# Optimization experiments

Hardware: AMD Instinct MI355X
Metric: run time of the kernel (lower is better)

The kernel has to match this reference:

```python
import jax, jax.numpy as jnp
import numpy as np

N = 50000
E = 1600000
INPUT_DIM = 128
HEADS = 4
OUT_DIM = 32
LRELU_ALPHA = 0.2


def setup_inputs() -> dict:
    key = jax.random.key(0)
    k1, k2, k3, k4, k5 = jax.random.split(key, 5)
    gain = 1.0 / (1.0 + LRELU_ALPHA)
    input_proj = jax.random.normal(k1, (N, INPUT_DIM), dtype=jnp.float32)
    edge_index = jax.random.randint(k2, (2, E), 0, N, dtype=jnp.int64)
    W = jax.random.normal(k3, (INPUT_DIM, HEADS * OUT_DIM), dtype=jnp.float32) * (gain / INPUT_DIM) ** 0.5
    A_left = jax.random.normal(k4, (HEADS, OUT_DIM, 1), dtype=jnp.float32) * (gain / OUT_DIM)
    A_right = jax.random.normal(k5, (HEADS, OUT_DIM, 1), dtype=jnp.float32) * (gain / OUT_DIM)
    return {"input_proj": input_proj, "edge_index": edge_index, "W": W, "A_left": A_left, "A_right": A_right}


def reference(input_proj, edge_index, W, A_left, A_right):
    n = input_proj.shape[0]
    heads, out_dim = A_left.shape[0], A_left.shape[1]
    # Linear projection: [N, heads, out_dim]
    H = (input_proj @ W).reshape(n, heads, out_dim)
    # Per-node attention scores: [N, heads]
    H_s = jnp.einsum('nhd,hd->nh', H, A_left[..., 0])
    H_t = jnp.einsum('nhd,hd->nh', H, A_right[..., 0])
    src = edge_index[0]
    tgt = edge_index[1]
    # Edge scores: leaky_relu(H_s[src] + H_t[tgt]) -> [E, heads]
    e = H_s[src] + H_t[tgt]
    e = jnp.where(e > 0, e, LRELU_ALPHA * e)
    # Segment softmax over neighborhoods keyed by source node (global max shift, as in original)
    e = jnp.exp(e - jnp.max(e))
    denom = jax.ops.segment_sum(e, src, num_segments=n)  # [N, heads]
    alpha = e / (denom[src] + 1e-8)
    # Weighted scatter-add aggregation of target features: [N, heads, out_dim]
    msg = alpha[:, :, None] * H[tgt]
    agg = jax.ops.segment_sum(msg, src, num_segments=n)
    # concat_last=True -> [N, heads*out_dim], then ELU
    res = agg.reshape(n, heads * out_dim)
    return jax.nn.elu(res)
```

## Files before the change

### kernel.cpp

```cpp
#include <hip/hip_runtime.h>

#define DIM 128
#define HEADS 4
#define ODIM 32
#define LRELU 0.2f
#define PT 4096
#define CAP 9216

typedef unsigned int u32;
typedef unsigned short u16;
typedef unsigned char u8;

typedef __attribute__((ext_vector_type(8))) short bf16x8;
typedef __attribute__((ext_vector_type(4))) float f32x4;

__device__ __forceinline__ u16 f2bf(float f) {
    union { u32 u; float f; } x; x.f = f;
    u32 u = x.u;
    u32 r = u + 0x7FFFu + ((u >> 16) & 1u);
    return (u16)(r >> 16);
}
__device__ __forceinline__ float blo(u32 b) {
    union { u32 u; float f; } x; x.u = b << 16; return x.f;
}
__device__ __forceinline__ float bhi(u32 b) {
    union { u32 u; float f; } x; x.u = b & 0xFFFF0000u; return x.f;
}

__global__ __launch_bounds__(256) void prep_kernel(
    const float* __restrict__ W, u16* __restrict__ Wt, int* __restrict__ bcur)
{
    __shared__ u16 s[128 * 136];
    int t = threadIdx.x;
    bcur[t] = t * CAP;
    for (int i = 0; i < 64; ++i) {
        int idx = i * 256 + t;
        int k = idx >> 7, nn = idx & 127;
        s[nn * 136 + k] = f2bf(W[idx]);
    }
    __syncthreads();
    for (int i = 0; i < 64; ++i) {
        int idx = i * 256 + t;
        int nn = idx >> 7, k = idx & 127;
        Wt[idx] = s[nn * 136 + k];
    }
}

__global__ __launch_bounds__(256) void proj_kernel(
    const float* __restrict__ X, const u16* __restrict__ Wt,
    const float* __restrict__ AL, const float* __restrict__ AR,
    u32* __restrict__ Hb, float* __restrict__ Hs, float* __restrict__ Ht, int n)
{
    __shared__ alignas(16) float sH[64 * 132];
    __shared__ float sAL[DIM], sAR[DIM];
    const int t = threadIdx.x;
    if (t < DIM) { sAL[t] = AL[t]; sAR[t] = AR[t]; }
    const int row0 = blockIdx.x * 64;
    const int w = t >> 6, lane = t & 63;
    const int quad = lane >> 4, nIdx = lane & 15;
    const int m = row0 + w * 16 + nIdx;

    f32x4 acc[8];
    #pragma unroll
    for (int c = 0; c < 8; ++c) acc[c] = (f32x4){0.f, 0.f, 0.f, 0.f};

    #pragma unroll
    for (int kq = 0; kq < 4; ++kq) {
        union { bf16x8 v; u16 e[8]; } a;
        if (m < n) {
            const float* xp = &X[(size_t)m * DIM + kq * 32 + quad * 8];
            float4 x0 = *(const float4*)xp;
            float4 x1 = *(const float4*)(xp + 4);
            a.e[0] = f2bf(x0.x); a.e[1] = f2bf(x0.y);
            a.e[2] = f2bf(x0.z); a.e[3] = f2bf(x0.w);
            a.e[4] = f2bf(x1.x); a.e[5] = f2bf(x1.y);
            a.e[6] = f2bf(x1.z); a.e[7] = f2bf(x1.w);
        } else {
            #pragma unroll
            for (int j = 0; j < 8; ++j) a.e[j] = 0;
        }
        #pragma unroll
        for (int c = 0; c < 8; ++c) {
            bf16x8 b = *(const bf16x8*)&Wt[(c * 16 + nIdx) * DIM + kq * 32 + quad * 8];
            acc[c] = __builtin_amdgcn_mfma_f32_16x16x32_bf16(a.v, b, acc[c], 0, 0, 0);
        }
    }
    #pragma unroll
    for (int c = 0; c < 8; ++c)
        #pragma unroll
        for (int r = 0; r < 4; ++r)
            sH[(w * 16 + quad * 4 + r) * 132 + c * 16 + nIdx] = acc[c][r];
    __syncthreads();

    #pragma unroll
    for (int i = 0; i < 16; ++i) {
        int idx = i * 256 + t;
        int r = idx >> 6, d2 = idx & 63;
        int gr = row0 + r;
        if (gr < n) {
            float2 hv = *(const float2*)&sH[r * 132 + 2 * d2];
            Hb[(size_t)gr * 64 + d2] = ((u32)f2bf(hv.y) << 16) | (u32)f2bf(hv.x);
        }
    }
    {
        int r = t >> 2, h = t & 3;
        float s = 0.f, s2 = 0.f;
        #pragma unroll
        for (int q = 0; q < ODIM; q += 4) {
            float4 hv = *(const float4*)&sH[r * 132 + h * ODIM + q];
            s  += hv.x*sAL[h*ODIM+q] + hv.y*sAL[h*ODIM+q+1] + hv.z*sAL[h*ODIM+q+2] + hv.w*sAL[h*ODIM+q+3];
            s2 += hv.x*sAR[h*ODIM+q] + hv.y*sAR[h*ODIM+q+1] + hv.z*sAR[h*ODIM+q+2] + hv.w*sAR[h*ODIM+q+3];
        }
        int gr = row0 + r;
        if (gr < n) { Hs[gr * HEADS + h] = s; Ht[gr * HEADS + h] = s2; }
    }
}

__device__ __forceinline__ int scan256_excl(int v, int t, int* wsum) {
    int lane = t & 63, w = t >> 6;
    int inc = v;
    #pragma unroll
    for (int ofs = 1; ofs < 64; ofs <<= 1) {
        int x = __shfl_up(inc, ofs);
        if (lane >= ofs) inc += x;
    }
    __syncthreads();
    if (lane == 63) wsum[w] = inc;
    __syncthreads();
    int add = 0;
    #pragma unroll
    for (int j = 0; j < 4; ++j) add += (j < w) ? wsum[j] : 0;
    return inc - v + add;
}

__global__ __launch_bounds__(256) void partition_kernel(
    const int* __restrict__ ei, int* __restrict__ bcur,
    u32* __restrict__ part, int E, int n)
{
    __shared__ u32 stage[PT];
    __shared__ u8  sbkt[PT];
    __shared__ int lcnt4[4][256];
    __shared__ int lcur4[4][256];
    __shared__ int loff[256], ltot[256], gbase[256];
    __shared__ int wsum[4];
    const int t = threadIdx.x;
    const int wv = t >> 6;
    const int base = blockIdx.x * PT;
    lcnt4[0][t] = 0; lcnt4[1][t] = 0; lcnt4[2][t] = 0; lcnt4[3][t] = 0;
    __syncthreads();

    u32 key[16];
    int bkt[16];
    #pragma unroll
    for (int i = 0; i < 16; ++i) {
        int e = base + i * 256 + t;
        bkt[i] = -1;
        key[i] = 0;
        if (e < E) {
            int src = ei[e];
            int tgt = ei[E + e];
            src = max(0, min(src, n - 1));
            tgt = max(0, min(tgt, n - 1));
            bkt[i] = src >> 8;
            key[i] = ((u32)(src & 255) << 17) | (u32)tgt;
            atomicAdd(&lcnt4[wv][bkt[i]], 1);
        }
    }
    __syncthreads();
    int c0 = lcnt4[0][t], c1 = lcnt4[1][t], c2 = lcnt4[2][t], c3 = lcnt4[3][t];
    int total = c0 + c1 + c2 + c3;
    int ex = scan256_excl(total, t, wsum);
    loff[t] = ex;
    ltot[t] = total;
    lcur4[0][t] = ex;
    lcur4[1][t] = ex + c0;
    lcur4[2][t] = ex + c0 + c1;
    lcur4[3][t] = ex + c0 + c1 + c2;
    gbase[t] = (total > 0) ? atomicAdd(&bcur[t], total) : 0;
    __syncthreads();
    #pragma unroll
    for (int i = 0; i < 16; ++i) {
        if (bkt[i] >= 0) {
            int p = atomicAdd(&lcur4[wv][bkt[i]], 1);
            stage[p] = key[i];
            sbkt[p] = (u8)bkt[i];
        }
    }
    __syncthreads();
    int tot = loff[255] + ltot[255];
    for (int i = t; i < tot; i += 256) {
        int b = sbkt[i];
        int dst = gbase[b] + (i - loff[b]);
        if (dst < (b + 1) * CAP) part[dst] = stage[i];
    }
}

__global__ __launch_bounds__(256) void csrfill_kernel(
    const u32* __restrict__ part, const int* __restrict__ bcur,
    int* __restrict__ off, int* __restrict__ csr_tgt, int n, int ntiles)
{
    __shared__ int lc4[4][256];
    __shared__ int lcur4[4][256];
    __shared__ int lo[256];
    __shared__ int wsum[4];
    __shared__ int sBase, sCnt;
    const int b = blockIdx.x, t = threadIdx.x;
    const int wv = t >> 6;
    int myc = (t < ntiles) ? (bcur[t] - t * CAP) : 0;
    myc = max(0, min(myc, CAP));
    int ex = scan256_excl(myc, t, wsum);
    if (t == b) { sBase = ex; sCnt = myc; }
    lc4[0][t] = 0; lc4[1][t] = 0; lc4[2][t] = 0; lc4[3][t] = 0;
    __syncthreads();
    const int pbase = b * CAP;
    const int base = sBase, cnt = sCnt;
    for (int i = t; i < cnt; i += 256)
        atomicAdd(&lc4[wv][part[pbase + i] >> 17], 1);
    __syncthreads();
    int c0 = lc4[0][t], c1 = lc4[1][t], c2 = lc4[2][t], c3 = lc4[3][t];
    int total = c0 + c1 + c2 + c3;
    int ex2 = scan256_excl(total, t, wsum);
    lo[t] = ex2;
    lcur4[0][t] = ex2;
    lcur4[1][t] = ex2 + c0;
    lcur4[2][t] = ex2 + c0 + c1;
    lcur4[3][t] = ex2 + c0 + c1 + c2;
    __syncthreads();
    int node = b * 256 + t;
    if (node < n) off[node] = base + lo[t];
    if (b == ntiles - 1 && t == 0) off[n] = base + cnt;
    for (int i = t; i < cnt; i += 256) {
        u32 key = part[pbase + i];
        int p = atomicAdd(&lcur4[wv][key >> 17], 1);
        csr_tgt[base + p] = (int)(key & 0x1FFFFu);
    }
}

__global__ __launch_bounds__(256) void agg_kernel(
    const u32* __restrict__ Hb, const float* __restrict__ Hs,
    const float* __restrict__ Ht, const int* __restrict__ off,
    const int* __restrict__ csr_tgt, float2* __restrict__ out, int n, int E)
{
    int node = (blockIdx.x * 256 + threadIdx.x) >> 6;
    int L = threadIdx.x & 63;
    if (node >= n) return;
    int lo = off[node], hi = off[node + 1];
    lo = max(0, min(lo, E));
    hi = max(lo, min(hi, E));
    const int h = L >> 4;
    const int eSel = (L & 31) >> 2;
    const int hSel = L & 3;
    float4 hs4 = *(const float4*)&Hs[node * HEADS];
    float hsC = hSel == 0 ? hs4.x : hSel == 1 ? hs4.y : hSel == 2 ? hs4.z : hs4.w;
    float hsO = h == 0 ? hs4.x : h == 1 ? hs4.y : h == 2 ? hs4.z : hs4.w;
    float ax = 0.f, ay = 0.f, Sd = 0.f, Srem = 0.f;

    int i = lo;
    for (; i + 8 <= hi; i += 8) {
        int tt[8];
        #pragma unroll
        for (int j = 0; j < 8; ++j) tt[j] = csr_tgt[i + j];
        int tsel = csr_tgt[i + eSel];
        float e = hsC + Ht[tsel * HEADS + hSel];
        float w = __expf(fminf(e > 0.f ? e : LRELU * e, 30.f));
        Sd += w;
        u32 bb[8];
        #pragma unroll
        for (int j = 0; j < 8; ++j) bb[j] = Hb[tt[j] * 64 + L];
        #pragma unroll
        for (int j = 0; j < 8; ++j) {
            float wj = __shfl(w, (j << 2) | h);
            ax += wj * blo(bb[j]);
            ay += wj * bhi(bb[j]);
        }
    }
    for (; i < hi; ++i) {
        int tgt = csr_tgt[i];
        float e = hsO + Ht[tgt * HEADS + h];
        float w = __expf(fminf(e > 0.f ? e : LRELU * e, 30.f));
        u32 b = Hb[tgt * 64 + L];
        ax += w * blo(b);
        ay += w * bhi(b);
        Srem += w;
    }
    float S = Srem;
    #pragma unroll
    for (int j = 0; j < 8; ++j) S += __shfl(Sd, (j << 2) | h);
    float inv = 1.f / (S + 1e-8f);
    float ox = ax * inv, oy = ay * inv;
    ox = ox > 0.f ? ox : (__expf(ox) - 1.f);
    oy = oy > 0.f ? oy : (__expf(oy) - 1.f);
    out[(size_t)node * 64 + L] = {ox, oy};
}

extern "C" void kernel_launch(void* const* d_in, const int* in_sizes, int n_in,
                              void* d_out, int out_size, void* d_ws, size_t ws_size,
                              hipStream_t stream) {
    const float* X  = (const float*)d_in[0];
    const int*   EI = (const int*)d_in[1];
    const float* W  = (const float*)d_in[2];
    const float* AL = (const float*)d_in[3];
    const float* AR = (const float*)d_in[4];
    const int n = in_sizes[0] / DIM;
    const int E = in_sizes[1] / 2;
    const int ntiles = (n + 255) / 256;

    char* ws = (char*)d_ws;
    size_t o = 0;
    auto alloc = [&](size_t bytes) -> void* {
        o = (o + 255) & ~(size_t)255;
        void* p = ws + o;
        o += bytes;
        return p;
    };
    int*   bcur    = (int*)alloc(256 * 4);
    u16*   Wt      = (u16*)alloc((size_t)DIM * DIM * 2);
    int*   off     = (int*)alloc((size_t)(n + 1) * 4);
    float* Hs      = (float*)alloc((size_t)n * HEADS * 4);
    float* Ht      = (float*)alloc((size_t)n * HEADS * 4);
    int*   csr_tgt = (int*)alloc((size_t)E * 4);
    u32*   part    = (u32*)alloc((size_t)ntiles * CAP * 4);
    u32*   Hb      = (u32*)alloc((size_t)n * 64 * 4);

    prep_kernel<<<1, 256, 0, stream>>>(W, Wt, bcur);
    proj_kernel<<<(n + 63) / 64, 256, 0, stream>>>(X, Wt, AL, AR, Hb, Hs, Ht, n);
    partition_kernel<<<(E + PT - 1) / PT, 256, 0, stream>>>(EI, bcur, part, E, n);
    csrfill_kernel<<<ntiles, 256, 0, stream>>>(part, bcur, off, csr_tgt, n, ntiles);
    agg_kernel<<<(n + 3) / 4, 256, 0, stream>>>(
        Hb, Hs, Ht, off, csr_tgt, (float2*)d_out, n, E);
}
```

Before: 205.7 us.

## Fuse projection and partition into one launch, split csrfill and prep across blocks

```diff
diff --git a/kernel.cpp b/kernel.cpp
--- a/kernel.cpp
+++ b/kernel.cpp
@@ -27,35 +27,122 @@
     union { u32 u; float f; } x; x.u = b & 0xFFFF0000u; return x.f;
 }
 
+__device__ __forceinline__ int scan256_excl(int v, int t, int* wsum) {
+    int lane = t & 63, w = t >> 6;
+    int inc = v;
+    #pragma unroll
+    for (int ofs = 1; ofs < 64; ofs <<= 1) {
+        int x = __shfl_up(inc, ofs);
+        if (lane >= ofs) inc += x;
+    }
+    __syncthreads();
+    if (lane == 63) wsum[w] = inc;
+    __syncthreads();
+    int add = 0;
+    #pragma unroll
+    for (int j = 0; j < 4; ++j) add += (j < w) ? wsum[j] : 0;
+    return inc - v + add;
+}
+
 __global__ __launch_bounds__(256) void prep_kernel(
     const float* __restrict__ W, u16* __restrict__ Wt, int* __restrict__ bcur)
 {
-    __shared__ u16 s[128 * 136];
-    int t = threadIdx.x;
-    bcur[t] = t * CAP;
-    for (int i = 0; i < 64; ++i) {
+    __shared__ u16 s[128 * 17];
+    const int t = threadIdx.x;
+    const int b = blockIdx.x;
+    if (b == 0) bcur[t] = t * CAP;
+    #pragma unroll
+    for (int i = 0; i < 8; ++i) {
         int idx = i * 256 + t;
-        int k = idx >> 7, nn = idx & 127;
-        s[nn * 136 + k] = f2bf(W[idx]);
-    }
-    __syncthreads();
-    for (int i = 0; i < 64; ++i) {
+        int kk = idx >> 7;
+        int nn = idx & 127;
+        s[nn * 17 + kk] = f2bf(W[(b * 16 + kk) * 128 + nn]);
+    }
+    __syncthreads();
+    #pragma unroll
+    for (int i = 0; i < 8; ++i) {
         int idx = i * 256 + t;
-        int nn = idx >> 7, k = idx & 127;
-        Wt[idx] = s[nn * 136 + k];
-    }
-}
-
-__global__ __launch_bounds__(256) void proj_kernel(
-    const float* __restrict__ X, const u16* __restrict__ Wt,
+        int nn = idx >> 4;
+        int kk = idx & 15;
+        Wt[nn * 128 + b * 16 + kk] = s[nn * 17 + kk];
+    }
+}
+
+__device__ __forceinline__ void partition_body(
+    char* smem, int bid, const int* __restrict__ ei, int* __restrict__ bcur,
+    u32* __restrict__ part, int E, int n)
+{
+    u32* stage = (u32*)smem;
+    u8*  sbkt  = (u8*)(smem + 16384);
+    int (*lcnt4)[256] = (int (*)[256])(smem + 20480);
+    int (*lcur4)[256] = (int (*)[256])(smem + 24576);
+    int* loff  = (int*)(smem + 28672);
+    int* ltot  = (int*)(smem + 29696);
+    int* gbase = (int*)(smem + 30720);
+    int* wsum  = (int*)(smem + 31744);
+    const int t = threadIdx.x;
+    const int wv = t >> 6;
+    const int base = bid * PT;
+    lcnt4[0][t] = 0; lcnt4[1][t] = 0; lcnt4[2][t] = 0; lcnt4[3][t] = 0;
+    __syncthreads();
+
+    u32 key[16];
+    int bkt[16];
+    #pragma unroll
+    for (int i = 0; i < 16; ++i) {
+        int e = base + i * 256 + t;
+        bkt[i] = -1;
+        key[i] = 0;
+        if (e < E) {
+            int src = ei[e];
+            int tgt = ei[E + e];
+            src = max(0, min(src, n - 1));
+            tgt = max(0, min(tgt, n - 1));
+            bkt[i] = src >> 8;
+            key[i] = ((u32)(src & 255) << 17) | (u32)tgt;
+            atomicAdd(&lcnt4[wv][bkt[i]], 1);
+        }
+    }
+    __syncthreads();
+    int c0 = lcnt4[0][t], c1 = lcnt4[1][t], c2 = lcnt4[2][t], c3 = lcnt4[3][t];
+    int total = c0 + c1 + c2 + c3;
+    int ex = scan256_excl(total, t, wsum);
+    loff[t] = ex;
+    ltot[t] = total;
+    lcur4[0][t] = ex;
+    lcur4[1][t] = ex + c0;
+    lcur4[2][t] = ex + c0 + c1;
+    lcur4[3][t] = ex + c0 + c1 + c2;
+    gbase[t] = (total > 0) ? atomicAdd(&bcur[t], total) : 0;
+    __syncthreads();
+    #pragma unroll
+    for (int i = 0; i < 16; ++i) {
+        if (bkt[i] >= 0) {
+            int p = atomicAdd(&lcur4[wv][bkt[i]], 1);
+            stage[p] = key[i];
+            sbkt[p] = (u8)bkt[i];
+        }
+    }
+    __syncthreads();
+    int tot = loff[255] + ltot[255];
+    for (int i = t; i < tot; i += 256) {
+        int b = sbkt[i];
+        int dst = gbase[b] + (i - loff[b]);
+        if (dst < (b + 1) * CAP) part[dst] = stage[i];
+    }
+}
+
+__device__ __forceinline__ void proj_body(
+    char* smem, int bid, const float* __restrict__ X, const u16* __restrict__ Wt,
     const float* __restrict__ AL, const float* __restrict__ AR,
     u32* __restrict__ Hb, float* __restrict__ Hs, float* __restrict__ Ht, int n)
 {
-    __shared__ alignas(16) float sH[64 * 132];
-    __shared__ float sAL[DIM], sAR[DIM];
+    float* sH  = (float*)smem;
+    float* sAL = (float*)(smem + 33792);
+    float* sAR = (float*)(smem + 34304);
     const int t = threadIdx.x;
     if (t < DIM) { sAL[t] = AL[t]; sAR[t] = AR[t]; }
-    const int row0 = blockIdx.x * 64;
+    const int row0 = bid * 64;
     const int w = t >> 6, lane = t & 63;
     const int quad = lane >> 4, nIdx = lane & 15;
     const int m = row0 + w * 16 + nIdx;
@@ -116,123 +203,69 @@
     }
 }
 
-__device__ __forceinline__ int scan256_excl(int v, int t, int* wsum) {
-    int lane = t & 63, w = t >> 6;
-    int inc = v;
-    #pragma unroll
-    for (int ofs = 1; ofs < 64; ofs <<= 1) {
-        int x = __shfl_up(inc, ofs);
-        if (lane >= ofs) inc += x;
-    }
-    __syncthreads();
-    if (lane == 63) wsum[w] = inc;
-    __syncthreads();
-    int add = 0;
-    #pragma unroll
-    for (int j = 0; j < 4; ++j) add += (j < w) ? wsum[j] : 0;
-    return inc - v + add;
-}
-
-__global__ __launch_bounds__(256) void partition_kernel(
-    const int* __restrict__ ei, int* __restrict__ bcur,
-    u32* __restrict__ part, int E, int n)
-{
-    __shared__ u32 stage[PT];
-    __shared__ u8  sbkt[PT];
-    __shared__ int lcnt4[4][256];
-    __shared__ int lcur4[4][256];
-    __shared__ int loff[256], ltot[256], gbase[256];
-    __shared__ int wsum[4];
-    const int t = threadIdx.x;
-    const int wv = t >> 6;
-    const int base = blockIdx.x * PT;
-    lcnt4[0][t] = 0; lcnt4[1][t] = 0; lcnt4[2][t] = 0; lcnt4[3][t] = 0;
-    __syncthreads();
-
-    u32 key[16];
-    int bkt[16];
-    #pragma unroll
-    for (int i = 0; i < 16; ++i) {
-        int e = base + i * 256 + t;
-        bkt[i] = -1;
-        key[i] = 0;
-        if (e < E) {
-            int src = ei[e];
-            int tgt = ei[E + e];
-            src = max(0, min(src, n - 1));
-            tgt = max(0, min(tgt, n - 1));
-            bkt[i] = src >> 8;
-            key[i] = ((u32)(src & 255) << 17) | (u32)tgt;
-            atomicAdd(&lcnt4[wv][bkt[i]], 1);
-        }
-    }
-    __syncthreads();
-    int c0 = lcnt4[0][t], c1 = lcnt4[1][t], c2 = lcnt4[2][t], c3 = lcnt4[3][t];
-    int total = c0 + c1 + c2 + c3;
-    int ex = scan256_excl(total, t, wsum);
-    loff[t] = ex;
-    ltot[t] = total;
-    lcur4[0][t] = ex;
-    lcur4[1][t] = ex + c0;
-    lcur4[2][t] = ex + c0 + c1;
-    lcur4[3][t] = ex + c0 + c1 + c2;
-    gbase[t] = (total > 0) ? atomicAdd(&bcur[t], total) : 0;
-    __syncthreads();
-    #pragma unroll
-    for (int i = 0; i < 16; ++i) {
-        if (bkt[i] >= 0) {
-            int p = atomicAdd(&lcur4[wv][bkt[i]], 1);
-            stage[p] = key[i];
-            sbkt[p] = (u8)bkt[i];
-        }
-    }
-    __syncthreads();
-    int tot = loff[255] + ltot[255];
-    for (int i = t; i < tot; i += 256) {
-        int b = sbkt[i];
-        int dst = gbase[b] + (i - loff[b]);
-        if (dst < (b + 1) * CAP) part[dst] = stage[i];
-    }
+__global__ __launch_bounds__(256) void fused_pp_kernel(
+    const float* __restrict__ X, const u16* __restrict__ Wt,
+    const float* __restrict__ AL, const float* __restrict__ AR,
+    u32* __restrict__ Hb, float* __restrict__ Hs, float* __restrict__ Ht,
+    const int* __restrict__ ei, int* __restrict__ bcur, u32* __restrict__ part,
+    int n, int E, int partBlocks)
+{
+    __shared__ alignas(16) char smem[34816];
+    if ((int)blockIdx.x < partBlocks)
+        partition_body(smem, blockIdx.x, ei, bcur, part, E, n);
+    else
+        proj_body(smem, blockIdx.x - partBlocks, X, Wt, AL, AR, Hb, Hs, Ht, n);
 }
 
 __global__ __launch_bounds__(256) void csrfill_kernel(
     const u32* __restrict__ part, const int* __restrict__ bcur,
     int* __restrict__ off, int* __restrict__ csr_tgt, int n, int ntiles)
 {
-    __shared__ int lc4[4][256];
-    __shared__ int lcur4[4][256];
-    __shared__ int lo[256];
+    __shared__ int lc4[4][128];
+    __shared__ int lcur4[4][128];
     __shared__ int wsum[4];
     __shared__ int sBase, sCnt;
-    const int b = blockIdx.x, t = threadIdx.x;
+    const int blk = blockIdx.x, t = threadIdx.x;
+    const int b = blk >> 1, half = blk & 1;
     const int wv = t >> 6;
     int myc = (t < ntiles) ? (bcur[t] - t * CAP) : 0;
     myc = max(0, min(myc, CAP));
     int ex = scan256_excl(myc, t, wsum);
     if (t == b) { sBase = ex; sCnt = myc; }
-    lc4[0][t] = 0; lc4[1][t] = 0; lc4[2][t] = 0; lc4[3][t] = 0;
+    if (t < 128) { lc4[0][t] = 0; lc4[1][t] = 0; lc4[2][t] = 0; lc4[3][t] = 0; }
     __syncthreads();
     const int pbase = b * CAP;
     const int base = sBase, cnt = sCnt;
-    for (int i = t; i < cnt; i += 256)
-        atomicAdd(&lc4[wv][part[pbase + i] >> 17], 1);
-    __syncthreads();
-    int c0 = lc4[0][t], c1 = lc4[1][t], c2 = lc4[2][t], c3 = lc4[3][t];
-    int total = c0 + c1 + c2 + c3;
+    for (int i = t; i < cnt; i += 256) {
+        int node8 = part[pbase + i] >> 17;
+        if ((node8 >> 7) == half) atomicAdd(&lc4[wv][node8 & 127], 1);
+    }
+    __syncthreads();
+    int c0 = 0, c1 = 0, c2 = 0, c3 = 0, total = 0;
+    if (t < 128) {
+        c0 = lc4[0][t]; c1 = lc4[1][t]; c2 = lc4[2][t]; c3 = lc4[3][t];
+        total = c0 + c1 + c2 + c3;
+    }
     int ex2 = scan256_excl(total, t, wsum);
-    lo[t] = ex2;
-    lcur4[0][t] = ex2;
-    lcur4[1][t] = ex2 + c0;
-    lcur4[2][t] = ex2 + c0 + c1;
-    lcur4[3][t] = ex2 + c0 + c1 + c2;
-    __syncthreads();
-    int node = b * 256 + t;
-    if (node < n) off[node] = base + lo[t];
-    if (b == ntiles - 1 && t == 0) off[n] = base + cnt;
+    int halfTot = wsum[0] + wsum[1];
+    int myBase = base + (half ? (cnt - halfTot) : 0);
+    if (t < 128) {
+        lcur4[0][t] = ex2;
+        lcur4[1][t] = ex2 + c0;
+        lcur4[2][t] = ex2 + c0 + c1;
+        lcur4[3][t] = ex2 + c0 + c1 + c2;
+        int node = b * 256 + half * 128 + t;
+        if (node < n) off[node] = myBase + ex2;
+    }
+    if (b == ntiles - 1 && half == 0 && t == 0) off[n] = base + cnt;
+    __syncthreads();
     for (int i = t; i < cnt; i += 256) {
         u32 key = part[pbase + i];
-        int p = atomicAdd(&lcur4[wv][key >> 17], 1);
-        csr_tgt[base + p] = (int)(key & 0x1FFFFu);
+        int node8 = key >> 17;
+        if ((node8 >> 7) == half) {
+            int p = atomicAdd(&lcur4[wv][node8 & 127], 1);
+            csr_tgt[myBase + p] = (int)(key & 0x1FFFFu);
+        }
     }
 }
 
@@ -322,10 +355,13 @@
     u32*   part    = (u32*)alloc((size_t)ntiles * CAP * 4);
     u32*   Hb      = (u32*)alloc((size_t)n * 64 * 4);
 
-    prep_kernel<<<1, 256, 0, stream>>>(W, Wt, bcur);
-    proj_kernel<<<(n + 63) / 64, 256, 0, stream>>>(X, Wt, AL, AR, Hb, Hs, Ht, n);
-    partition_kernel<<<(E + PT - 1) / PT, 256, 0, stream>>>(EI, bcur, part, E, n);
-    csrfill_kernel<<<ntiles, 256, 0, stream>>>(part, bcur, off, csr_tgt, n, ntiles);
+    const int PB = (E + PT - 1) / PT;
+    const int JB = (n + 63) / 64;
+
+    prep_kernel<<<8, 256, 0, stream>>>(W, Wt, bcur);
+    fused_pp_kernel<<<PB + JB, 256, 0, stream>>>(
+        X, Wt, AL, AR, Hb, Hs, Ht, EI, bcur, part, n, E, PB);
+    csrfill_kernel<<<ntiles * 2, 256, 0, stream>>>(part, bcur, off, csr_tgt, n, ntiles);
     agg_kernel<<<(n + 3) / 4, 256, 0, stream>>>(
         Hb, Hs, Ht, off, csr_tgt, (float2*)d_out, n, E);
 }
```

After: 194.3 us. 1.06x faster.
